# Kernel optimization log

Hardware: AMD Instinct MI355X
Metric: run time of the kernel (lower is better)

The kernel has to match this reference:

```python
import jax, jax.numpy as jnp
import numpy as np

NUM_HEADS = 4
DROPOUT_P_X = 0.1
DROPOUT_P_LQ = 0.3


def setup_inputs() -> dict:
    key = jax.random.key(0)
    ks = jax.random.split(key, 7)
    d_in, d_out = 128, 128
    b, t, n = 4, 32, 288
    s = 1.0 / np.sqrt(d_in)
    return {
        "x": jax.random.normal(ks[0], (b, t, n, d_in), dtype=jnp.float32),
        "Wq": jax.random.normal(ks[1], (d_in, d_out), dtype=jnp.float32) * s,
        "Wk": jax.random.normal(ks[2], (d_in, d_out), dtype=jnp.float32) * s,
        "Wv": jax.random.normal(ks[3], (d_in, d_out), dtype=jnp.float32) * s,
        "Wo": jax.random.normal(ks[4], (d_out, d_out), dtype=jnp.float32) * s,
        "bo": jnp.zeros((d_out,), dtype=jnp.float32),
        "drop_u": jax.random.uniform(ks[5], (b, t, NUM_HEADS, n, n), dtype=jnp.float32),
        "num_x_tokens": 256,
    }


def reference(x, Wq, Wk, Wv, Wo, bo, drop_u, num_x_tokens):
    b, t, n, d_in = x.shape
    d_out = Wq.shape[1]
    H = NUM_HEADS
    hd = d_out // H

    # QKV projections (Linear without bias: x @ W, W stored (d_in, d_out))
    def heads(y):
        return y.reshape(b, t, n, H, hd).transpose(0, 1, 3, 2, 4)  # (b,t,H,n,hd)

    q = heads(x @ Wq)
    k = heads(x @ Wk)
    v = heads(x @ Wv)

    scores = jnp.einsum("bthqd,bthkd->bthqk", q, k) / jnp.sqrt(jnp.asarray(hd, x.dtype))
    w = jax.nn.softmax(scores, axis=-1)  # (b,t,H,n,n)

    # Block-wise differential dropout (training mode), deterministic via drop_u.
    keep_x = 1.0 - DROPOUT_P_X
    keep_lq = 1.0 - DROPOUT_P_LQ
    is_x = jnp.arange(n) < num_x_tokens  # (n,)
    # keep prob per (query, key) position: x-x block uses keep_x, all others keep_lq
    keep_p = jnp.where(is_x[:, None] & is_x[None, :], keep_x, keep_lq)  # (n,n)
    mask = (drop_u < keep_p).astype(w.dtype)

    n_xx = num_x_tokens * num_x_tokens
    n_total = n * n
    expected_kept = n_xx * keep_x + (n_total - n_xx) * keep_lq
    scale = n_total / expected_kept

    w = w * mask * jnp.asarray(scale, w.dtype)

    ctx = jnp.einsum("bthqk,bthkd->bthqd", w, v)
    ctx = ctx.transpose(0, 1, 3, 2, 4).reshape(b, t, n, d_out)
    return ctx @ Wo + bo
```

## Files before the change

kernel.cpp:

```cpp
#include <hip/hip_runtime.h>
#include <hip/hip_bf16.h>
#include <cstdint>
#include <cstddef>

typedef __bf16 bf16_t;
typedef __bf16 bf16x8 __attribute__((ext_vector_type(8)));
typedef __bf16 bf16x4 __attribute__((ext_vector_type(4)));
typedef float f32x4 __attribute__((ext_vector_type(4)));

#define B_   4
#define T_   32
#define N_   288
#define D_   128
#define H_   4
#define HD_  32
#define BT_  (B_*T_)
#define NTOK (BT_*N_)
#define BTH  (BT_*H_)

#define OFF_Q   ((size_t)0)
#define OFF_K   (OFF_Q  + (size_t)BTH*N_*HD_*2)
#define OFF_VT  (OFF_K  + (size_t)BTH*N_*HD_*2)
#define OFF_CTX (OFF_VT + (size_t)BTH*N_*HD_*2)
#define OFF_WT  (OFF_CTX + (size_t)NTOK*D_*2)

__global__ __launch_bounds__(256) void prep_weights(
    const float* __restrict__ Wq, const float* __restrict__ Wk,
    const float* __restrict__ Wv, const float* __restrict__ Wo,
    bf16_t* __restrict__ Wt) {
  int idx = blockIdx.x * 256 + threadIdx.x;
  int m   = idx >> 14;
  int rem = idx & 16383;
  int col = rem >> 7;
  int k   = rem & 127;
  const float* W = (m == 0) ? Wq : (m == 1) ? Wk : (m == 2) ? Wv : Wo;
  Wt[m * 16384 + col * 128 + k] = (bf16_t)W[k * 128 + col];
}

__global__ __launch_bounds__(256) void qkv_proj(
    const float* __restrict__ x, const bf16_t* __restrict__ Wt,
    bf16_t* __restrict__ Q, bf16_t* __restrict__ K, bf16_t* __restrict__ VT) {
  const int lane = threadIdx.x & 63;
  const int wid  = threadIdx.x >> 6;
  const int lr   = lane & 15, lg = lane >> 4;
  const int tokbase = blockIdx.x * 64 + wid * 16;

  bf16x8 a[4];
  const float* xr = x + (size_t)(tokbase + lr) * D_ + lg * 8;
#pragma unroll
  for (int ks = 0; ks < 4; ++ks) {
    float4 f0 = *reinterpret_cast<const float4*>(xr + ks * 32);
    float4 f1 = *reinterpret_cast<const float4*>(xr + ks * 32 + 4);
    bf16x8 v;
    v[0] = (bf16_t)f0.x; v[1] = (bf16_t)f0.y; v[2] = (bf16_t)f0.z; v[3] = (bf16_t)f0.w;
    v[4] = (bf16_t)f1.x; v[5] = (bf16_t)f1.y; v[6] = (bf16_t)f1.z; v[7] = (bf16_t)f1.w;
    a[ks] = v;
  }

  const int tok0 = tokbase + lg * 4;
  const int bt   = tok0 / N_;
  const int n0   = tok0 - bt * N_;

#pragma unroll
  for (int m = 0; m < 3; ++m) {
    const bf16_t* Wm = Wt + m * 16384;
#pragma unroll
    for (int ct = 0; ct < 8; ++ct) {
      const int col = ct * 16 + lr;
      f32x4 acc = {0.f, 0.f, 0.f, 0.f};
#pragma unroll
      for (int ks = 0; ks < 4; ++ks) {
        bf16x8 b = *reinterpret_cast<const bf16x8*>(Wm + col * D_ + ks * 32 + lg * 8);
        acc = __builtin_amdgcn_mfma_f32_16x16x32_bf16(a[ks], b, acc, 0, 0, 0);
      }
      const int h = col >> 5, dh = col & 31;
      if (m == 2) {
        bf16x4 pk;
        pk[0] = (bf16_t)acc[0]; pk[1] = (bf16_t)acc[1];
        pk[2] = (bf16_t)acc[2]; pk[3] = (bf16_t)acc[3];
        *reinterpret_cast<bf16x4*>(
            VT + ((size_t)(bt * H_ + h) * HD_ + dh) * N_ + n0) = pk;
      } else {
        bf16_t* P = (m == 0) ? Q : K;
        size_t base = ((size_t)(bt * H_ + h) * N_ + n0) * HD_ + dh;
        P[base]           = (bf16_t)acc[0];
        P[base + HD_]     = (bf16_t)acc[1];
        P[base + 2 * HD_] = (bf16_t)acc[2];
        P[base + 3 * HD_] = (bf16_t)acc[3];
      }
    }
  }
}

__global__ __launch_bounds__(384, 2) void attn(
    const bf16_t* __restrict__ Q, const bf16_t* __restrict__ K,
    const bf16_t* __restrict__ VT, const float* __restrict__ drop_u,
    const int* __restrict__ nxp, bf16_t* __restrict__ CTX) {
  __shared__ bf16_t wlds[6][16][104];
  __shared__ unsigned long long mbits64[1296];

  const int lane = threadIdx.x & 63;
  const int wid  = threadIdx.x >> 6;
  const int lr   = lane & 15, lg = lane >> 4;
  const int bth  = blockIdx.x;
  const int bt   = bth >> 2, h = bth & 3;

  const int   nx    = *nxp;
  const float keepx = 1.0f - 0.1f;
  const float keepl = 1.0f - 0.3f;
  const float nxx   = (float)nx * (float)nx;
  const float ntot  = (float)(N_ * N_);
  const float dropscale = ntot / (nxx * keepx + (ntot - nxx) * keepl);
  const float sc = 0.17677669529663687f;

  const bf16_t* Qh = Q  + (size_t)bth * N_ * HD_;
  const bf16_t* Kh = K  + (size_t)bth * N_ * HD_;
  const bf16_t* Vh = VT + (size_t)bth * HD_ * N_;
  const float*  Uh = drop_u + (size_t)bth * N_ * N_;

  {
    const float* Uw = Uh + wid * 13824;
    const int rowbase = wid * 48;
#pragma unroll 1
    for (int g = 0; g < 24; ++g) {
      float u[9];
#pragma unroll
      for (int e = 0; e < 9; ++e) u[e] = Uw[g * 576 + e * 64 + lane];
#pragma unroll
      for (int e = 0; e < 9; ++e) {
        int off = e * 64 + lane;
        int rin = off >= 288 ? 1 : 0;
        int col = off - rin * 288;
        int row = rowbase + g * 2 + rin;
        float kp = (row < nx && col < nx) ? keepx : keepl;
        unsigned long long bal = __ballot(u[e] < kp);
        if (lane == 0) mbits64[wid * 216 + g * 9 + e] = bal;
      }
    }
  }
  __syncthreads();
  const unsigned int* mb = (const unsigned int*)mbits64;

  for (int ti = 0; ti < 3; ++ti) {
    const int tile    = wid + ti * 6;
    const int rowbase = tile * 16;

    bf16x8 a = *reinterpret_cast<const bf16x8*>(Qh + (rowbase + lr) * HD_ + lg * 8);
    f32x4 acc[18];
#pragma unroll
    for (int ct = 0; ct < 18; ++ct) {
      bf16x8 b = *reinterpret_cast<const bf16x8*>(Kh + (ct * 16 + lr) * HD_ + lg * 8);
      f32x4 z = {0.f, 0.f, 0.f, 0.f};
      acc[ct] = __builtin_amdgcn_mfma_f32_16x16x32_bf16(a, b, z, 0, 0, 0);
    }

    float m[4] = {-1e30f, -1e30f, -1e30f, -1e30f};
#pragma unroll
    for (int ct = 0; ct < 18; ++ct)
#pragma unroll
      for (int r = 0; r < 4; ++r) m[r] = fmaxf(m[r], acc[ct][r]);
#pragma unroll
    for (int i = 1; i < 16; i <<= 1)
#pragma unroll
      for (int r = 0; r < 4; ++r) m[r] = fmaxf(m[r], __shfl_xor(m[r], i));

    const int q0 = rowbase + lg * 4;
    float s[4];
#pragma unroll
    for (int r = 0; r < 4; ++r) {
      float acc_s = 0.f;
      unsigned int rd[9];
#pragma unroll
      for (int w9 = 0; w9 < 9; ++w9) rd[w9] = mb[(q0 + r) * 9 + w9];
#pragma unroll
      for (int ct = 0; ct < 18; ++ct) {
        float e = __expf((acc[ct][r] - m[r]) * sc);
        acc_s += e;
        unsigned int bit = (rd[ct >> 1] >> ((ct & 1) * 16 + lr)) & 1u;
        acc[ct][r] = bit ? e : 0.f;
      }
      s[r] = acc_s;
    }
#pragma unroll
    for (int i = 1; i < 16; i <<= 1)
#pragma unroll
      for (int r = 0; r < 4; ++r) s[r] += __shfl_xor(s[r], i);

    float inv[4];
#pragma unroll
    for (int r = 0; r < 4; ++r) inv[r] = dropscale / s[r];

    f32x4 cd[2] = {{0.f,0.f,0.f,0.f},{0.f,0.f,0.f,0.f}};
#pragma unroll
    for (int chunk = 0; chunk < 3; ++chunk) {
#pragma unroll
      for (int cc = 0; cc < 6; ++cc) {
        const int ct = chunk * 6 + cc;
#pragma unroll
        for (int r = 0; r < 4; ++r)
          wlds[wid][lg * 4 + r][cc * 16 + lr] = (bf16_t)(acc[ct][r] * inv[r]);
      }
#pragma unroll
      for (int dt = 0; dt < 2; ++dt)
#pragma unroll
        for (int k3 = 0; k3 < 3; ++k3) {
          bf16x8 aw = *reinterpret_cast<const bf16x8*>(&wlds[wid][lr][k3 * 32 + lg * 8]);
          bf16x8 bv = *reinterpret_cast<const bf16x8*>(
              Vh + (dt * 16 + lr) * N_ + chunk * 96 + k3 * 32 + lg * 8);
          cd[dt] = __builtin_amdgcn_mfma_f32_16x16x32_bf16(aw, bv, cd[dt], 0, 0, 0);
        }
    }

#pragma unroll
    for (int dt = 0; dt < 2; ++dt) {
      size_t obase = ((size_t)bt * N_ + q0) * D_ + h * HD_ + dt * 16 + lr;
#pragma unroll
      for (int r = 0; r < 4; ++r)
        CTX[obase + (size_t)r * D_] = (bf16_t)cd[dt][r];
    }
  }
}

__global__ __launch_bounds__(256) void out_proj(
    const bf16_t* __restrict__ CTX, const bf16_t* __restrict__ Wt,
    const float* __restrict__ bo, float* __restrict__ out) {
  const int lane = threadIdx.x & 63;
  const int wid  = threadIdx.x >> 6;
  const int lr   = lane & 15, lg = lane >> 4;
  const int tokbase = blockIdx.x * 64 + wid * 16;
  const bf16_t* Wo = Wt + 3 * 16384;

  bf16x8 a[4];
#pragma unroll
  for (int ks = 0; ks < 4; ++ks)
    a[ks] = *reinterpret_cast<const bf16x8*>(
        CTX + (size_t)(tokbase + lr) * D_ + ks * 32 + lg * 8);

  const int tok0 = tokbase + lg * 4;
#pragma unroll
  for (int ct = 0; ct < 8; ++ct) {
    const int col = ct * 16 + lr;
    f32x4 acc = {0.f, 0.f, 0.f, 0.f};
#pragma unroll
    for (int ks = 0; ks < 4; ++ks) {
      bf16x8 b = *reinterpret_cast<const bf16x8*>(Wo + col * D_ + ks * 32 + lg * 8);
      acc = __builtin_amdgcn_mfma_f32_16x16x32_bf16(a[ks], b, acc, 0, 0, 0);
    }
    const float bias = bo[col];
    size_t ob = (size_t)tok0 * D_ + col;
#pragma unroll
    for (int r = 0; r < 4; ++r) out[ob + (size_t)r * D_] = acc[r] + bias;
  }
}

extern "C" void kernel_launch(void* const* d_in, const int* in_sizes, int n_in,
                              void* d_out, int out_size, void* d_ws, size_t ws_size,
                              hipStream_t stream) {
  (void)in_sizes; (void)n_in; (void)out_size; (void)ws_size;
  const float* x  = (const float*)d_in[0];
  const float* Wq = (const float*)d_in[1];
  const float* Wk = (const float*)d_in[2];
  const float* Wv = (const float*)d_in[3];
  const float* Wo = (const float*)d_in[4];
  const float* bo = (const float*)d_in[5];
  const float* du = (const float*)d_in[6];
  const int*   nx = (const int*)d_in[7];

  char* ws = (char*)d_ws;
  bf16_t* Qb   = (bf16_t*)(ws + OFF_Q);
  bf16_t* Kb   = (bf16_t*)(ws + OFF_K);
  bf16_t* VTb  = (bf16_t*)(ws + OFF_VT);
  bf16_t* CTXb = (bf16_t*)(ws + OFF_CTX);
  bf16_t* Wt   = (bf16_t*)(ws + OFF_WT);

  prep_weights<<<256, 256, 0, stream>>>(Wq, Wk, Wv, Wo, Wt);
  qkv_proj<<<NTOK / 64, 256, 0, stream>>>(x, Wt, Qb, Kb, VTb);
  attn<<<BTH, 384, 0, stream>>>(Qb, Kb, VTb, du, nx, CTXb);
  out_proj<<<NTOK / 64, 256, 0, stream>>>(CTXb, Wt, bo, (float*)d_out);
}
```

Measured before the change: 355.7 us.

## Precompute dropout bitmask in a separate kernel and load it in attention

Moves the conversion of drop_u into packed keep-bits out of the attention kernel into a standalone build_mask kernel that writes the bits to workspace. The attention kernel then only copies the compact bitmask into LDS instead of streaming the full float drop_u tensor. The aim is to get better memory parallelism on the bandwidth-heavy drop_u read, since the attention grid is small (512 blocks). It costs an extra kernel launch and a workspace round trip for the mask, and drop_u still has to be read in full.

```diff
diff --git a/kernel.cpp b/kernel.cpp
--- a/kernel.cpp
+++ b/kernel.cpp
@@ -23,6 +23,7 @@
 #define OFF_VT  (OFF_K  + (size_t)BTH*N_*HD_*2)
 #define OFF_CTX (OFF_VT + (size_t)BTH*N_*HD_*2)
 #define OFF_WT  (OFF_CTX + (size_t)NTOK*D_*2)
+#define OFF_MB  (OFF_WT + (size_t)4*128*128*2)
 
 __global__ __launch_bounds__(256) void prep_weights(
     const float* __restrict__ Wq, const float* __restrict__ Wk,
@@ -35,6 +36,38 @@
   int k   = rem & 127;
   const float* W = (m == 0) ? Wq : (m == 1) ? Wk : (m == 2) ? Wv : Wo;
   Wt[m * 16384 + col * 128 + k] = (bf16_t)W[k * 128 + col];
+}
+
+__global__ __launch_bounds__(256) void build_mask(
+    const float* __restrict__ drop_u, const int* __restrict__ nxp,
+    unsigned long long* __restrict__ maskG) {
+  const int lane = threadIdx.x & 63;
+  const int wv   = (blockIdx.x * 256 + threadIdx.x) >> 6;
+  const int nx   = *nxp;
+  const float keepx = 0.9f, keepl = 0.7f;
+#pragma unroll 1
+  for (int it = 0; it < 9; ++it) {
+    const int p    = wv * 9 + it;
+    const int rowg = (p % 144) * 2;
+    const float* Up = drop_u + (size_t)p * 576;
+    float u[9];
+#pragma unroll
+    for (int e = 0; e < 9; ++e) u[e] = Up[e * 64 + lane];
+    unsigned long long bal[9];
+#pragma unroll
+    for (int e = 0; e < 9; ++e) {
+      int off = e * 64 + lane;
+      int rin = off >= 288 ? 1 : 0;
+      int col = off - rin * 288;
+      int row = rowg + rin;
+      float kp = (row < nx && col < nx) ? keepx : keepl;
+      bal[e] = __ballot(u[e] < kp);
+    }
+    if (lane == 0) {
+#pragma unroll
+      for (int e = 0; e < 9; ++e) maskG[(size_t)p * 9 + e] = bal[e];
+    }
+  }
 }
 
 __global__ __launch_bounds__(256) void qkv_proj(
@@ -94,7 +127,7 @@
 
 __global__ __launch_bounds__(384, 2) void attn(
     const bf16_t* __restrict__ Q, const bf16_t* __restrict__ K,
-    const bf16_t* __restrict__ VT, const float* __restrict__ drop_u,
+    const bf16_t* __restrict__ VT, const unsigned long long* __restrict__ maskG,
     const int* __restrict__ nxp, bf16_t* __restrict__ CTX) {
   __shared__ bf16_t wlds[6][16][104];
   __shared__ unsigned long long mbits64[1296];
@@ -116,27 +149,11 @@
   const bf16_t* Qh = Q  + (size_t)bth * N_ * HD_;
   const bf16_t* Kh = K  + (size_t)bth * N_ * HD_;
   const bf16_t* Vh = VT + (size_t)bth * HD_ * N_;
-  const float*  Uh = drop_u + (size_t)bth * N_ * N_;
 
   {
-    const float* Uw = Uh + wid * 13824;
-    const int rowbase = wid * 48;
-#pragma unroll 1
-    for (int g = 0; g < 24; ++g) {
-      float u[9];
-#pragma unroll
-      for (int e = 0; e < 9; ++e) u[e] = Uw[g * 576 + e * 64 + lane];
-#pragma unroll
-      for (int e = 0; e < 9; ++e) {
-        int off = e * 64 + lane;
-        int rin = off >= 288 ? 1 : 0;
-        int col = off - rin * 288;
-        int row = rowbase + g * 2 + rin;
-        float kp = (row < nx && col < nx) ? keepx : keepl;
-        unsigned long long bal = __ballot(u[e] < kp);
-        if (lane == 0) mbits64[wid * 216 + g * 9 + e] = bal;
-      }
-    }
+    const unsigned int* mg = (const unsigned int*)maskG + (size_t)bth * 2592;
+    unsigned int* md = (unsigned int*)mbits64;
+    for (int i = threadIdx.x; i < 2592; i += 384) md[i] = mg[i];
   }
   __syncthreads();
   const unsigned int* mb = (const unsigned int*)mbits64;
@@ -272,9 +289,11 @@
   bf16_t* VTb  = (bf16_t*)(ws + OFF_VT);
   bf16_t* CTXb = (bf16_t*)(ws + OFF_CTX);
   bf16_t* Wt   = (bf16_t*)(ws + OFF_WT);
-
+  unsigned long long* maskG = (unsigned long long*)(ws + OFF_MB);
+
+  build_mask<<<2048, 256, 0, stream>>>(du, nx, maskG);
   prep_weights<<<256, 256, 0, stream>>>(Wq, Wk, Wv, Wo, Wt);
   qkv_proj<<<NTOK / 64, 256, 0, stream>>>(x, Wt, Qb, Kb, VTb);
-  attn<<<BTH, 384, 0, stream>>>(Qb, Kb, VTb, du, nx, CTXb);
+  attn<<<BTH, 384, 0, stream>>>(Qb, Kb, VTb, maskG, nx, CTXb);
   out_proj<<<NTOK / 64, 256, 0, stream>>>(CTXb, Wt, bo, (float*)d_out);
 }
```

New measurement: 361.7 us. About the same (+1.7%).
